# Performance work log

Hardware: AMD Instinct MI355X
Metric: run time of the kernel (lower is better)

Reference implementation:

```python
import jax, jax.numpy as jnp
import numpy as np

SLOPE = 0.01  # torch nn.LeakyReLU default negative_slope
K = 2


def setup_inputs() -> dict:
    key = jax.random.key(0)
    ks = jax.random.split(key, 5)
    B, D, E = 65536, 256, 16
    s = 0.02
    return {
        "x": jax.random.normal(ks[0], (B, D), jnp.float32),
        "Wr1": jax.random.normal(ks[1], (D, D), jnp.float32) * s,
        "br1": jnp.zeros((D,), jnp.float32),
        "Wr2": jax.random.normal(ks[2], (E, D), jnp.float32) * s,
        "br2": jnp.zeros((E,), jnp.float32),
        "We": jax.random.normal(ks[3], (E, D, D), jnp.float32) * s,
        "be": jnp.zeros((E, D), jnp.float32),
    }


def reference(x, Wr1, br1, Wr2, br2, We, be):
    # Router: MLP [D -> D -> E] with LeakyReLU between layers
    h = jax.nn.leaky_relu(x @ Wr1.T + br1, SLOPE)          # [B, D]
    logits = h @ Wr2.T + br2                               # [B, E]
    top_vals, top_idx = jax.lax.top_k(logits, K)           # [B, K]
    probs = jax.nn.softmax(top_vals, axis=-1)              # [B, K]
    # Dense per-expert linears (matches torch: all experts computed)
    expert_out = jnp.einsum('bi,eoi->beo', x, We) + be     # [B, E, O]
    # Gather the top-k experts' outputs
    sel = jnp.take_along_axis(expert_out, top_idx[:, :, None], axis=1)  # [B, K, O]
    out = jnp.einsum('bko,bk->bo', sel, probs)             # [B, O]
    return jax.nn.leaky_relu(out, SLOPE)
```

## Files before the change

kernel.cpp:

```cpp
#include <hip/hip_runtime.h>

typedef unsigned short ushort_t;
typedef __attribute__((ext_vector_type(8))) __bf16 bf16x8;
typedef __attribute__((ext_vector_type(4))) float f32x4;

#define MARGIN 1.5e-3f
#define FT 4

__device__ __forceinline__ float bf2f(ushort_t u){
  union { unsigned int i; float f; } v; v.i = ((unsigned int)u) << 16; return v.f;
}
__device__ __forceinline__ ushort_t f2bf(float f){
  union { float f; unsigned int i; } v; v.f = f;
  unsigned int x = v.i;
  return (ushort_t)((x + 0x7fffu + ((x >> 16) & 1u)) >> 16);
}
__device__ __forceinline__ void async_load16(const void* g, void* l){
  __builtin_amdgcn_global_load_lds((const __attribute__((address_space(1))) void*)g,
                                   (__attribute__((address_space(3))) void*)l, 16, 0, 0);
}

__global__ __launch_bounds__(256) void k_prep(const float* __restrict__ We,
    const float* __restrict__ Wr1, const float* __restrict__ Wr2,
    ushort_t* __restrict__ WebP, ushort_t* __restrict__ W1b,
    ushort_t* __restrict__ W2h, ushort_t* __restrict__ W2l,
    float* __restrict__ Wr1T, float* __restrict__ Wr2T)
{
  int idx = blockIdx.x*256 + threadIdx.x;
  if (idx < 1048576){
    int n = (idx >> 8) & 255, k = idx & 255;
    int dst = (idx & ~65535) + ((n>>4)<<12) + ((k>>3)<<7) + ((n&15)<<3) + (k&7);
    WebP[dst] = f2bf(We[idx]);
  }
  if (idx < 65536){
    W1b[idx] = f2bf(Wr1[idx]);
    int k = idx >> 8, o = idx & 255;
    Wr1T[idx] = Wr1[o*256 + k];
  }
  if (idx < 4096){
    float w = Wr2[idx];
    ushort_t wh = f2bf(w);
    W2h[idx] = wh;
    W2l[idx] = f2bf(w - bf2f(wh));
    int k = idx >> 4, e = idx & 15;
    Wr2T[idx] = Wr2[e*256 + k];
  }
}

__global__ __launch_bounds__(256) void r1r2_fused(const float* __restrict__ x,
    const ushort_t* __restrict__ W1b, const float* __restrict__ br1,
    const ushort_t* __restrict__ W2h, const ushort_t* __restrict__ W2l,
    const float* __restrict__ br2,
    int* __restrict__ pid, float2* __restrict__ pAB,
    int* __restrict__ fixCnt, int* __restrict__ fixTok)
{
  __shared__ __align__(16) char smem[46336];
  ushort_t* As = (ushort_t*)smem;
  char*     Bs = smem + 9216;
  ushort_t* hB = (ushort_t*)smem;
  float*    lg = (float*)(smem + 41984);
  const int tid = threadIdx.x;
  const int wave = tid>>6, lane = tid&63, q = lane>>4, col = lane&15;
  const int tok0 = blockIdx.x*64;

  f32x4 acc[4][4];
  #pragma unroll
  for (int i=0;i<4;i++)
    #pragma unroll
    for (int j=0;j<4;j++) acc[i][j] = f32x4{0.f,0.f,0.f,0.f};

  for (int kc = 0; kc < 4; ++kc){
    const int kb = kc*64;
    __syncthreads();
    f32x4 xv[2][2];
    #pragma unroll
    for (int j=0;j<2;j++){
      int idx = j*256 + tid, row = idx>>3, c8 = idx&7;
      xv[j][0] = *(const f32x4*)&x[(tok0+row)*256 + kb + c8*8];
      xv[j][1] = *(const f32x4*)&x[(tok0+row)*256 + kb + c8*8 + 4];
    }
    #pragma unroll
    for (int i=0;i<8;i++){
      int r0 = wave*64 + i*8;
      int grow = r0 + (lane>>3);
      int kc8 = (lane&7) ^ (grow&7);
      async_load16(W1b + grow*256 + kb + kc8*8, Bs + r0*128);
    }
    #pragma unroll
    for (int j=0;j<2;j++){
      int idx = j*256 + tid, row = idx>>3, c8 = idx&7;
      union { uint4 u; ushort_t s[8]; } pk;
      pk.s[0]=f2bf(xv[j][0][0]); pk.s[1]=f2bf(xv[j][0][1]); pk.s[2]=f2bf(xv[j][0][2]); pk.s[3]=f2bf(xv[j][0][3]);
      pk.s[4]=f2bf(xv[j][1][0]); pk.s[5]=f2bf(xv[j][1][1]); pk.s[6]=f2bf(xv[j][1][2]); pk.s[7]=f2bf(xv[j][1][3]);
      *(uint4*)&As[row*72 + c8*8] = pk.u;
    }
    __syncthreads();
    #pragma unroll
    for (int kk=0;kk<2;kk++){
      bf16x8 a[4], b[4];
      #pragma unroll
      for (int rf=0;rf<4;rf++) a[rf] = *(const bf16x8*)&As[(rf*16+col)*72 + kk*32 + q*8];
      #pragma unroll
      for (int cf=0;cf<4;cf++){
        int n = wave*64 + cf*16 + col;
        b[cf] = *(const bf16x8*)(Bs + n*128 + (((kk*4+q) ^ (n&7))*16));
      }
      #pragma unroll
      for (int rf=0;rf<4;rf++)
        #pragma unroll
        for (int cf=0;cf<4;cf++)
          acc[rf][cf] = __builtin_amdgcn_mfma_f32_16x16x32_bf16(a[rf], b[cf], acc[rf][cf], 0,0,0);
    }
  }
  __syncthreads();
  {
    float br1v[4];
    #pragma unroll
    for (int cf=0;cf<4;cf++) br1v[cf] = br1[wave*64 + cf*16 + col];
    #pragma unroll
    for (int rf=0;rf<4;rf++)
      #pragma unroll
      for (int cf=0;cf<4;cf++){
        int o = wave*64 + cf*16 + col;
        #pragma unroll
        for (int r=0;r<4;r++){
          int row = rf*16 + q*4 + r;
          float p = acc[rf][cf][r] + br1v[cf];
          p = p > 0.f ? p : 0.01f*p;
          hB[row*264 + o] = f2bf(p);
        }
      }
  }
  __syncthreads();
  {
    f32x4 acc2 = f32x4{0.f,0.f,0.f,0.f};
    #pragma unroll
    for (int c2=0;c2<8;c2++){
      bf16x8 a2 = *(const bf16x8*)&hB[(wave*16+col)*264 + c2*32 + q*8];
      bf16x8 bh = *(const bf16x8*)&W2h[col*256 + c2*32 + q*8];
      bf16x8 bl = *(const bf16x8*)&W2l[col*256 + c2*32 + q*8];
      acc2 = __builtin_amdgcn_mfma_f32_16x16x32_bf16(a2, bh, acc2, 0,0,0);
      acc2 = __builtin_amdgcn_mfma_f32_16x16x32_bf16(a2, bl, acc2, 0,0,0);
    }
    #pragma unroll
    for (int r=0;r<4;r++) lg[(wave*16 + q*4 + r)*17 + col] = acc2[r];
  }
  __syncthreads();
  if (tid < 64){
    const int tok = tok0 + tid;
    float v[16];
    #pragma unroll
    for (int e=0;e<16;e++) v[e] = lg[tid*17 + e] + br2[e];
    float best=-3.4e38f, sec=-3.4e38f, thr=-3.4e38f; int b1=0, b2=0;
    #pragma unroll
    for (int e=0;e<16;e++){
      float val = v[e];
      if (val > best){ thr=sec; sec=best; b2=b1; best=val; b1=e; }
      else if (val > sec){ thr=sec; sec=val; b2=e; }
      else if (val > thr){ thr=val; }
    }
    float ex = expf(sec - best);
    float s = 1.f + ex;
    float p1 = 1.f/s, p2 = ex/s;
    int eA = b1 < b2 ? b1 : b2;
    int eB = b1 < b2 ? b2 : b1;
    float pA = b1 < b2 ? p1 : p2;
    float pB = b1 < b2 ? p2 : p1;
    pid[tok] = eA*16 + eB;
    pAB[tok] = make_float2(pA, pB);
    if (sec - thr < MARGIN){
      int slot = atomicAdd(fixCnt, 1);
      fixTok[slot] = tok;
    }
  }
}

__global__ __launch_bounds__(256) void k_fixup(const float* __restrict__ x,
    const float* __restrict__ Wr1T, const float* __restrict__ br1,
    const float* __restrict__ Wr2T, const float* __restrict__ br2,
    const int* __restrict__ fixCnt, const int* __restrict__ fixTok,
    int* __restrict__ pid, float2* __restrict__ pAB)
{
  __shared__ __align__(16) float xsT[256][FT];
  __shared__ double hs[FT*256];
  __shared__ double lg4[FT][16][4];
  const int tid = threadIdx.x;
  const int n = *fixCnt;
  for (int base = blockIdx.x*FT; base < n; base += gridDim.x*FT){
    const int nt = min(FT, n - base);
    __syncthreads();
    for (int i = tid; i < nt*256; i += 256){
      int t = i >> 8, c = i & 255;
      xsT[c][t] = x[fixTok[base + t]*256 + c];
    }
    __syncthreads();
    {
      const int o = tid;
      const float* wp = Wr1T + o;
      double a0=0, a1=0, a2=0, a3=0;
      float wbA[8], wbB[8];
      #pragma unroll
      for (int j=0;j<8;j++) wbA[j] = wp[j*256];
      #pragma unroll 1
      for (int g=0; g<32; g+=2){
        #pragma unroll
        for (int j=0;j<8;j++) wbB[j] = wp[((g+1)*8+j)*256];
        #pragma unroll
        for (int j=0;j<8;j++){
          double w = (double)wbA[j];
          f32x4 xv = *(const f32x4*)&xsT[g*8+j][0];
          a0 += (double)xv[0]*w;
          a1 += (double)xv[1]*w;
          a2 += (double)xv[2]*w;
          a3 += (double)xv[3]*w;
        }
        if (g+2 < 32){
          #pragma unroll
          for (int j=0;j<8;j++) wbA[j] = wp[((g+2)*8+j)*256];
        }
        #pragma unroll
        for (int j=0;j<8;j++){
          double w = (double)wbB[j];
          f32x4 xv = *(const f32x4*)&xsT[(g+1)*8+j][0];
          a0 += (double)xv[0]*w;
          a1 += (double)xv[1]*w;
          a2 += (double)xv[2]*w;
          a3 += (double)xv[3]*w;
        }
      }
      double b = (double)br1[o], v;
      v = a0+b; hs[0*256+o] = v>0.0 ? v : 0.01*v;
      v = a1+b; hs[1*256+o] = v>0.0 ? v : 0.01*v;
      v = a2+b; hs[2*256+o] = v>0.0 ? v : 0.01*v;
      v = a3+b; hs[3*256+o] = v>0.0 ? v : 0.01*v;
    }
    __syncthreads();
    {
      const int t = tid>>6, e = (tid>>2)&15, kq = tid&3;
      const double* hp = hs + t*256 + kq*64;
      const float*  w2 = Wr2T + kq*64*16 + e;
      double a0=0, a1=0;
      #pragma unroll 8
      for (int k=0;k<64;k+=2){
        a0 += hp[k]   * (double)w2[k*16];
        a1 += hp[k+1] * (double)w2[(k+1)*16];
      }
      lg4[t][e][kq] = a0 + a1;
    }
    __syncthreads();
    if (tid < FT*16){
      const int t = tid>>4, e = tid&15;
      lg4[t][e][0] = ((lg4[t][e][0]+lg4[t][e][1]) + (lg4[t][e][2]+lg4[t][e][3]))
                     + (double)br2[e];
    }
    __syncthreads();
    if (tid < nt){
      const int tok = fixTok[base + tid];
      double best=-1e300, sec=-1e300; int b1=0, b2=0;
      #pragma unroll
      for (int e=0;e<16;e++){
        double val = lg4[tid][e][0];
        if (val > best){ sec=best; b2=b1; best=val; b1=e; }
        else if (val > sec){ sec=val; b2=e; }
      }
      double ex = exp(sec - best);
      double s = 1.0 + ex;
      double p1 = 1.0/s, p2 = ex/s;
      int eA = b1 < b2 ? b1 : b2;
      int eB = b1 < b2 ? b2 : b1;
      float pA = (float)(b1 < b2 ? p1 : p2);
      float pB = (float)(b1 < b2 ? p2 : p1);
      pid[tok] = eA*16 + eB;
      pAB[tok] = make_float2(pA, pB);
    }
  }
}

__global__ __launch_bounds__(256) void k_hist(const int* __restrict__ pid, int* __restrict__ cnt)
{
  __shared__ int hc[256];
  const int tid = threadIdx.x;
  hc[tid] = 0; __syncthreads();
  atomicAdd(&hc[pid[blockIdx.x*256 + tid]], 1);
  __syncthreads();
  if (hc[tid]) atomicAdd(&cnt[tid], hc[tid]);
}

__global__ __launch_bounds__(256) void k_scan(int* __restrict__ cnt, int* __restrict__ cur,
    int* __restrict__ off, int* __restrict__ tileOff, int* __restrict__ tilePair)
{
  __shared__ int sc[256];
  const int tid = threadIdx.x;
  int c = cnt[tid];
  sc[tid] = c; __syncthreads();
  for (int s=1;s<256;s<<=1){ int v = (tid>=s)? sc[tid-s]:0; __syncthreads(); sc[tid]+=v; __syncthreads(); }
  int inc = sc[tid];
  off[tid] = inc - c;
  cur[tid] = inc - c;
  if (tid==255) off[256] = inc;
  int tc = (c+31)>>5;
  __syncthreads();
  sc[tid] = tc; __syncthreads();
  for (int s=1;s<256;s<<=1){ int v = (tid>=s)? sc[tid-s]:0; __syncthreads(); sc[tid]+=v; __syncthreads(); }
  tileOff[tid] = sc[tid] - tc;
  if (tid==255) tileOff[256] = sc[tid];
  int t0 = sc[tid] - tc;
  for (int i=0;i<tc;i++) tilePair[t0+i] = tid;
}

__global__ __launch_bounds__(256) void k_scatter(const int* __restrict__ pid,
    int* __restrict__ cur, int* __restrict__ sortedTok)
{
  int b = blockIdx.x*256 + threadIdx.x;
  int p = pid[b];
  int slot = atomicAdd(&cur[p], 1);
  sortedTok[slot] = b;
}

__global__ __launch_bounds__(256) void k_expert(const float* __restrict__ x,
    const ushort_t* __restrict__ WebP, const float* __restrict__ be,
    const int* __restrict__ off, const int* __restrict__ tileOff,
    const int* __restrict__ tilePair,
    const int* __restrict__ sortedTok, const float2* __restrict__ pAB,
    float* __restrict__ out)
{
  const int totTiles = tileOff[256];
  const int bid = blockIdx.x;
  if (bid >= totTiles) return;
  __shared__ __align__(16) char smem[34048];
  ushort_t* xtA = (ushort_t*)smem;
  ushort_t* xtB = (ushort_t*)(smem + 16384);
  __shared__ int toks[32];
  __shared__ float pAs[32], pBs[32];
  const int tid = threadIdx.x;
  const int p = tilePair[bid];
  const int tstart = off[p] + (bid - tileOff[p])*32;
  const int nt = min(32, off[p+1] - tstart);
  if (tid < 32){
    if (tid < nt){
      int t = sortedTok[tstart + tid];
      toks[tid] = t;
      float2 ab = pAB[t];
      pAs[tid] = ab.x; pBs[tid] = ab.y;
    } else { toks[tid] = -1; pAs[tid]=0.f; pBs[tid]=0.f; }
  }
  __syncthreads();

  #pragma unroll
  for (int j=0;j<4;j++){
    int ci = j*256 + tid, row = ci>>5, c = ci&31;
    int t = toks[row]; t = t < 0 ? 0 : t;
    float pA = pAs[row], pB = pBs[row];
    f32x4 v0 = *(const f32x4*)&x[t*256 + c*8];
    f32x4 v1 = *(const f32x4*)&x[t*256 + c*8 + 4];
    union { uint4 u; ushort_t s[8]; } pk;
    pk.s[0]=f2bf(v0[0]*pA); pk.s[1]=f2bf(v0[1]*pA); pk.s[2]=f2bf(v0[2]*pA); pk.s[3]=f2bf(v0[3]*pA);
    pk.s[4]=f2bf(v1[0]*pA); pk.s[5]=f2bf(v1[1]*pA); pk.s[6]=f2bf(v1[2]*pA); pk.s[7]=f2bf(v1[3]*pA);
    *(uint4*)&xtA[row*256 + ((c ^ (row&7))<<3)] = pk.u;
    pk.s[0]=f2bf(v0[0]*pB); pk.s[1]=f2bf(v0[1]*pB); pk.s[2]=f2bf(v0[2]*pB); pk.s[3]=f2bf(v0[3]*pB);
    pk.s[4]=f2bf(v1[0]*pB); pk.s[5]=f2bf(v1[1]*pB); pk.s[6]=f2bf(v1[2]*pB); pk.s[7]=f2bf(v1[3]*pB);
    *(uint4*)&xtB[row*256 + ((c ^ (row&7))<<3)] = pk.u;
  }
  __syncthreads();

  const int wave = tid>>6, lane = tid&63, q = lane>>4, col = lane&15;
  const int eA = p >> 4, eB = p & 15;

  float pa_r[8], pb_r[8];
  #pragma unroll
  for (int rf=0;rf<2;rf++)
    #pragma unroll
    for (int r=0;r<4;r++){
      int row = rf*16 + q*4 + r;
      pa_r[rf*4+r] = pAs[row]; pb_r[rf*4+r] = pBs[row];
    }
  f32x4 acc[2][4];
  #pragma unroll
  for (int cf=0;cf<4;cf++){
    int o = wave*64 + cf*16 + col;
    float bA_ = be[eA*256 + o], bB_ = be[eB*256 + o];
    #pragma unroll
    for (int rf=0;rf<2;rf++)
      #pragma unroll
      for (int r=0;r<4;r++)
        acc[rf][cf][r] = pa_r[rf*4+r]*bA_ + pb_r[rf*4+r]*bB_;
  }

  const ushort_t* bAp = WebP + eA*65536 + (wave*4)*4096 + q*128 + col*8;
  const ushort_t* bBp = WebP + eB*65536 + (wave*4)*4096 + q*128 + col*8;

  bf16x8 bufA[3][4], bufB[3][4];
  #pragma unroll
  for (int cf=0;cf<4;cf++){
    bufA[0][cf] = *(const bf16x8*)&bAp[cf*4096];
    bufB[0][cf] = *(const bf16x8*)&bBp[cf*4096];
  }
  #pragma unroll
  for (int cf=0;cf<4;cf++){
    bufA[1][cf] = *(const bf16x8*)&bAp[cf*4096 + 512];
    bufB[1][cf] = *(const bf16x8*)&bBp[cf*4096 + 512];
  }
  #pragma unroll
  for (int s=0;s<8;s++){
    const int cb = s % 3;
    if (s < 6){
      const int nb = (s+2) % 3;
      #pragma unroll
      for (int cf=0;cf<4;cf++){
        bufA[nb][cf] = *(const bf16x8*)&bAp[cf*4096 + (s+2)*512];
        bufB[nb][cf] = *(const bf16x8*)&bBp[cf*4096 + (s+2)*512];
      }
    }
    const int k8 = 4*s + q;
    bf16x8 aA[2], aB[2];
    #pragma unroll
    for (int rf=0;rf<2;rf++){
      aA[rf] = *(const bf16x8*)&xtA[(rf*16+col)*256 + ((k8 ^ (col&7))<<3)];
      aB[rf] = *(const bf16x8*)&xtB[(rf*16+col)*256 + ((k8 ^ (col&7))<<3)];
    }
    #pragma unroll
    for (int cf=0;cf<4;cf++){
      #pragma unroll
      for (int rf=0;rf<2;rf++)
        acc[rf][cf] = __builtin_amdgcn_mfma_f32_16x16x32_bf16(aA[rf], bufA[cb][cf], acc[rf][cf], 0,0,0);
      #pragma unroll
      for (int rf=0;rf<2;rf++)
        acc[rf][cf] = __builtin_amdgcn_mfma_f32_16x16x32_bf16(aB[rf], bufB[cb][cf], acc[rf][cf], 0,0,0);
    }
  }

  float* obuf = (float*)smem;
  __syncthreads();
  #pragma unroll
  for (int cf=0;cf<4;cf++){
    int o = wave*64 + cf*16 + col;
    #pragma unroll
    for (int rf=0;rf<2;rf++)
      #pragma unroll
      for (int r=0;r<4;r++){
        int row = rf*16 + q*4 + r;
        float v = acc[rf][cf][r];
        v = v > 0.f ? v : 0.01f*v;
        obuf[row*264 + o] = v;
      }
  }
  __syncthreads();
  #pragma unroll
  for (int j=0;j<8;j++){
    int idx = j*256 + tid;
    int lrow = idx>>6, c4 = idx&63;
    int t = toks[lrow];
    if (t >= 0)
      *(f32x4*)&out[t*256 + c4*4] = *(const f32x4*)&obuf[lrow*264 + c4*4];
  }
}

extern "C" void kernel_launch(void* const* d_in, const int* in_sizes, int n_in,
                              void* d_out, int out_size, void* d_ws, size_t ws_size,
                              hipStream_t stream)
{
  const float* x   = (const float*)d_in[0];
  const float* Wr1 = (const float*)d_in[1];
  const float* br1 = (const float*)d_in[2];
  const float* Wr2 = (const float*)d_in[3];
  const float* br2 = (const float*)d_in[4];
  const float* We  = (const float*)d_in[5];
  const float* be  = (const float*)d_in[6];
  float* out = (float*)d_out;

  char* ws = (char*)d_ws;
  ushort_t* WebP     = (ushort_t*)ws;
  ushort_t* W1b      = (ushort_t*)(ws + 2097152);
  ushort_t* W2h      = (ushort_t*)(ws + 2228224);
  ushort_t* W2l      = (ushort_t*)(ws + 2236416);
  int*      pid      = (int*)(ws + 2244608);
  float2*   pAB      = (float2*)(ws + 2506752);
  int*      sortedTok= (int*)(ws + 3031040);
  int*      fixTok   = (int*)(ws + 3293184);
  int*      cnt      = (int*)(ws + 3555328);
  int*      fixCnt   = cnt + 256;
  int*      cur      = cnt + 272;
  int*      off      = cnt + 528;
  int*      tileOff  = cnt + 785;
  float*    Wr1T     = (float*)(ws + 3559504);
  float*    Wr2T     = (float*)(ws + 3821648);
  int*      tilePair = (int*)(ws + 3838032);

  hipMemsetAsync(cnt, 0, 257*sizeof(int), stream);
  k_prep    <<<4096, 256, 0, stream>>>(We, Wr1, Wr2, WebP, W1b, W2h, W2l, Wr1T, Wr2T);
  r1r2_fused<<<1024, 256, 0, stream>>>(x, W1b, br1, W2h, W2l, br2, pid, pAB, fixCnt, fixTok);
  k_fixup   <<<2048, 256, 0, stream>>>(x, Wr1T, br1, Wr2T, br2, fixCnt, fixTok, pid, pAB);
  k_hist    <<<256,  256, 0, stream>>>(pid, cnt);
  k_scan    <<<1,    256, 0, stream>>>(cnt, cur, off, tileOff, tilePair);
  k_scatter <<<256,  256, 0, stream>>>(pid, cur, sortedTok);
  k_expert  <<<2304, 256, 0, stream>>>(x, WebP, be, off, tileOff, tilePair, sortedTok, pAB, out);
}
```

Before: 297.3 us.

## Replace global-atomic token scatter with per-block histograms and column prefix scan

Token bucketing by expert pair no longer relies on global atomic counters. Each block now writes its own histogram into a transposed table. A new column-scan kernel turns that table into per-block prefix offsets and per-pair totals, and the scatter uses only shared-memory atomics plus those precomputed offsets. This removes contended global atomics and makes the token order within each bucket closer to ascending, at the cost of one extra kernel launch and a 256x256 histogram table round-trip.

```diff
diff --git a/kernel.cpp b/kernel.cpp
--- a/kernel.cpp
+++ b/kernel.cpp
@@ -276,17 +276,30 @@
   }
 }
 
-__global__ __launch_bounds__(256) void k_hist(const int* __restrict__ pid, int* __restrict__ cnt)
+__global__ __launch_bounds__(256) void k_hist(const int* __restrict__ pid,
+    int* __restrict__ blockHistT)
 {
   __shared__ int hc[256];
   const int tid = threadIdx.x;
   hc[tid] = 0; __syncthreads();
   atomicAdd(&hc[pid[blockIdx.x*256 + tid]], 1);
   __syncthreads();
-  if (hc[tid]) atomicAdd(&cnt[tid], hc[tid]);
-}
-
-__global__ __launch_bounds__(256) void k_scan(int* __restrict__ cnt, int* __restrict__ cur,
+  blockHistT[tid*256 + blockIdx.x] = hc[tid];
+}
+
+__global__ __launch_bounds__(256) void k_colscan(const int* __restrict__ blockHistT,
+    int* __restrict__ blockPre, int* __restrict__ cnt)
+{
+  __shared__ int sc[256];
+  const int p = blockIdx.x, b = threadIdx.x;
+  int v = blockHistT[p*256 + b];
+  sc[b] = v; __syncthreads();
+  for (int s=1;s<256;s<<=1){ int u = (b>=s)? sc[b-s]:0; __syncthreads(); sc[b]+=u; __syncthreads(); }
+  blockPre[b*256 + p] = sc[b] - v;
+  if (b == 255) cnt[p] = sc[255];
+}
+
+__global__ __launch_bounds__(256) void k_scan(const int* __restrict__ cnt,
     int* __restrict__ off, int* __restrict__ tileOff, int* __restrict__ tilePair)
 {
   __shared__ int sc[256];
@@ -296,7 +309,6 @@
   for (int s=1;s<256;s<<=1){ int v = (tid>=s)? sc[tid-s]:0; __syncthreads(); sc[tid]+=v; __syncthreads(); }
   int inc = sc[tid];
   off[tid] = inc - c;
-  cur[tid] = inc - c;
   if (tid==255) off[256] = inc;
   int tc = (c+31)>>5;
   __syncthreads();
@@ -309,12 +321,16 @@
 }
 
 __global__ __launch_bounds__(256) void k_scatter(const int* __restrict__ pid,
-    int* __restrict__ cur, int* __restrict__ sortedTok)
-{
-  int b = blockIdx.x*256 + threadIdx.x;
-  int p = pid[b];
-  int slot = atomicAdd(&cur[p], 1);
-  sortedTok[slot] = b;
+    const int* __restrict__ off, const int* __restrict__ blockPre,
+    int* __restrict__ sortedTok)
+{
+  __shared__ int lc[256];
+  const int tid = threadIdx.x, b = blockIdx.x;
+  lc[tid] = 0; __syncthreads();
+  int tok = b*256 + tid;
+  int p = pid[tok];
+  int local = atomicAdd(&lc[p], 1);
+  sortedTok[off[p] + blockPre[b*256 + p] + local] = tok;
 }
 
 __global__ __launch_bounds__(256) void k_expert(const float* __restrict__ x,
@@ -479,19 +495,21 @@
   int*      fixTok   = (int*)(ws + 3293184);
   int*      cnt      = (int*)(ws + 3555328);
   int*      fixCnt   = cnt + 256;
-  int*      cur      = cnt + 272;
   int*      off      = cnt + 528;
   int*      tileOff  = cnt + 785;
   float*    Wr1T     = (float*)(ws + 3559504);
   float*    Wr2T     = (float*)(ws + 3821648);
   int*      tilePair = (int*)(ws + 3838032);
-
-  hipMemsetAsync(cnt, 0, 257*sizeof(int), stream);
+  int*      blockHistT=(int*)(ws + 3854416);
+  int*      blockPre = (int*)(ws + 4116560);
+
+  hipMemsetAsync(fixCnt, 0, sizeof(int), stream);
   k_prep    <<<4096, 256, 0, stream>>>(We, Wr1, Wr2, WebP, W1b, W2h, W2l, Wr1T, Wr2T);
   r1r2_fused<<<1024, 256, 0, stream>>>(x, W1b, br1, W2h, W2l, br2, pid, pAB, fixCnt, fixTok);
   k_fixup   <<<2048, 256, 0, stream>>>(x, Wr1T, br1, Wr2T, br2, fixCnt, fixTok, pid, pAB);
-  k_hist    <<<256,  256, 0, stream>>>(pid, cnt);
-  k_scan    <<<1,    256, 0, stream>>>(cnt, cur, off, tileOff, tilePair);
-  k_scatter <<<256,  256, 0, stream>>>(pid, cur, sortedTok);
+  k_hist    <<<256,  256, 0, stream>>>(pid, blockHistT);
+  k_colscan <<<256,  256, 0, stream>>>(blockHistT, blockPre, cnt);
+  k_scan    <<<1,    256, 0, stream>>>(cnt, off, tileOff, tilePair);
+  k_scatter <<<256,  256, 0, stream>>>(pid, off, blockPre, sortedTok);
   k_expert  <<<2304, 256, 0, stream>>>(x, WebP, be, off, tileOff, tilePair, sortedTok, pAB, out);
 }
```

Result: faster. 242.1 us (-18.6%).
